# Optimization experiments

Measured on AMD Instinct MI355X. Metric: run time of the kernel, lower is better.

The kernel has to match this reference:

```python
import jax, jax.numpy as jnp
import numpy as np
import math

B, I, J = 4, 48, 384
D_TEXT, D_MEL, D_ATT = 512, 80, 128
NOISE_SCALE = 2.0
LOG_EPS = -1000.0


def setup_inputs() -> dict:
    key = jax.random.key(0)
    ks = jax.random.split(key, 8)
    return {
        "text_embeddings": jax.random.normal(ks[0], (B, I, D_TEXT), jnp.float32),
        "mel_embeddings": jax.random.normal(ks[1], (B, J, D_MEL), jnp.float32),
        "noise": jax.random.normal(ks[2], (B, I, J), jnp.float32),
        "W_text": jax.random.normal(ks[3], (D_TEXT, D_ATT), jnp.float32) * (1.0 / math.sqrt(D_TEXT)),
        "W_mel": jax.random.normal(ks[4], (D_MEL, D_ATT), jnp.float32) * (1.0 / math.sqrt(D_MEL)),
        "b_mel": jnp.zeros((D_ATT,), jnp.float32),
        "v_w": jax.random.normal(ks[5], (D_ATT,), jnp.float32) * math.sqrt(1.0 / D_ATT),
        "v_b": jnp.zeros((), jnp.float32),
        "text_mask": jnp.ones((B, I), bool),
        "mel_mask": jnp.ones((B, J), bool),
    }


def reference(text_embeddings, mel_embeddings, noise, W_text, W_mel, b_mel, v_w, v_b, text_mask, mel_mask):
    # ---- compute_energy: additive (Bahdanau) attention, v(tanh(Wt x_i + Wm m_j + b)) ----
    pt = text_embeddings @ W_text                    # (B,I,D_att), no bias
    pm = mel_embeddings @ W_mel + b_mel              # (B,J,D_att)
    energy = jnp.tanh(pt[:, :, None, :] + pm[:, None, :, :]) @ v_w + v_b   # (B,I,J)
    energy = energy + NOISE_SCALE * noise            # apply_noise

    tlen = text_mask.sum(1)                          # (B,)
    mlen = mel_mask.sum(1)                           # (B,)
    ii = jnp.arange(I)
    jj = jnp.arange(J)

    # ---- invalid mask for P(B_i = j | B_{i-1} = k): monotonic (j >= k), padding, force last ----
    inv = (jj[:, None] < jj[None, :])[None, None, :, :]                       # j < k invalid
    inv = inv | (~text_mask)[:, :, None, None]
    inv = inv | (~mel_mask)[:, None, :, None] | (~mel_mask)[:, None, None, :]
    last = (ii[None, :] == tlen[:, None] - 1)[:, :, None] & (jj[None, :] != mlen[:, None] - 1)[:, None, :]
    inv = inv | last[:, :, :, None]                                           # force_assign_last=True

    e4 = jnp.where(inv, LOG_EPS, energy[..., None])                           # (B,I,J,K)
    lcp = e4 - jax.nn.logsumexp(e4, axis=2, keepdims=True)                    # log P(j | i, k)
    geq = jax.lax.cumlogsumexp(lcp, axis=2, reverse=True)                     # log P(B_i >= j | k)
    geq = jnp.where(inv, LOG_EPS, geq)

    # ---- compute_forward_pass: banded DP over text positions (log domain) ----
    width = J - I + 2
    lcp_pad = jnp.concatenate([lcp, jnp.full((B, I, 1, J), LOG_EPS, lcp.dtype)], axis=2)  # (B,I,J+1,K)
    row0 = jnp.full((B, J + 1), -jnp.inf, lcp.dtype).at[:, 0].set(0.0)

    def step(prev, i):
        # B_ij[:, i, i : J-I+i+2] = LSE_k( B_ij[:, i-1, k] + lcp[:, i-1, i-1 : J-I+i+1, k] )
        blk = jax.lax.dynamic_slice(lcp_pad, (0, i - 1, i - 1, 0), (B, 1, width, J))[:, 0]  # (B,width,K)
        vals = jax.nn.logsumexp(prev[:, None, :-1] + blk, axis=2)                            # (B,width)
        row = jnp.full((B, J + 2), -jnp.inf, lcp.dtype)
        row = jax.lax.dynamic_update_slice(row, vals, (0, i))[:, :J + 1]
        return row, row

    _, rows = jax.lax.scan(step, row0, jnp.arange(1, I + 1))                  # (I,B,J+1)
    # Bij_forward = B_ij[:, :-1, :-1]
    Bij = jnp.concatenate([row0[:, None, :], jnp.moveaxis(rows, 0, 1)[:, :I - 1]], axis=1)[:, :, :-1]  # (B,I,J)

    # ---- compute_interval_probability: soft[b,i,j] = LSE_k( Bij[b,i,k] + geq[b,i,j,k] ) ----
    soft = jax.nn.logsumexp(Bij[:, :, None, :] + geq, axis=3)                 # (B,I,J)

    expanded = jnp.einsum('bij,bid->bjd', jnp.exp(soft), text_embeddings)     # (B,J,D_text)
    return soft, expanded
```

## Files before the change

### kernel.cpp

```cpp
#include <hip/hip_runtime.h>
#include <hip/hip_bf16.h>
#include <math.h>

#define B_ 4
#define I_ 48
#define J_ 384
#define DT_ 512
#define DM_ 80
#define DA_ 128
#define WIDTH_ 338
#define NEG (-1e30f)
#define LOG2E 1.4426950408889634f
#define LN2 0.6931471805599453f
#define LOGEPS2 (-1442.6950408889634f)
#define VPT 6

typedef float f32x4 __attribute__((ext_vector_type(4)));
typedef float f32x2 __attribute__((ext_vector_type(2)));

__device__ __forceinline__ float fexp2(float x) { return __builtin_amdgcn_exp2f(x); }
__device__ __forceinline__ float flog2(float x) { return __builtin_amdgcn_logf(x); }

template<int CTRL, int RMASK>
__device__ __forceinline__ float dppf(float x) {
    return __int_as_float(__builtin_amdgcn_update_dpp(
        __float_as_int(NEG), __float_as_int(x), CTRL, RMASK, 0xF, false));
}
__device__ __forceinline__ float rlane(float x, int l) {
    return __int_as_float(__builtin_amdgcn_readlane(__float_as_int(x), l));
}

__device__ __forceinline__ float lse2(float a, float b) {
    float m = fmaxf(a, b);
    float d = a - b;
    return m + flog2(1.0f + fexp2(-fabsf(d)));
}

__device__ __forceinline__ float wave_scan_fwd(float x) {
    x = lse2(x, dppf<0x111, 0xF>(x));
    x = lse2(x, dppf<0x112, 0xF>(x));
    x = lse2(x, dppf<0x114, 0xF>(x));
    x = lse2(x, dppf<0x118, 0xF>(x));
    x = lse2(x, dppf<0x142, 0xA>(x));
    x = lse2(x, dppf<0x143, 0xC>(x));
    return x;
}
__device__ __forceinline__ float wave_scan_rev(float x, int lane) {
    x = lse2(x, dppf<0x101, 0xF>(x));
    x = lse2(x, dppf<0x102, 0xF>(x));
    x = lse2(x, dppf<0x104, 0xF>(x));
    x = lse2(x, dppf<0x108, 0xF>(x));
    float s16 = rlane(x, 16), s32 = rlane(x, 32), s48 = rlane(x, 48);
    float a  = lse2(s32, s48);
    float b2 = lse2(s16, a);
    int row = lane >> 4;
    float pre = (row == 0) ? b2 : (row == 1) ? a : (row == 2) ? s48 : NEG;
    return lse2(x, pre);
}

__device__ __forceinline__ float tanh_fast(float x) {
    float t = fexp2(x * (2.0f * LOG2E));
    return fmaf(-2.0f, __builtin_amdgcn_rcpf(t + 1.0f), 1.0f);
}

__global__ __launch_bounds__(128) void proj_kernel(
        const float* __restrict__ text, const float* __restrict__ mel,
        const float* __restrict__ Wt, const float* __restrict__ Wm,
        const float* __restrict__ bm, float* __restrict__ pt, float* __restrict__ pm) {
    int blk = blockIdx.x;
    int d = threadIdx.x;
    __shared__ float sx[DT_];
    if (blk < B_ * I_) {
        const float* x = text + blk * DT_;
        for (int e = d; e < DT_; e += DA_) sx[e] = x[e];
        __syncthreads();
        float acc = 0.f;
        #pragma unroll 8
        for (int e = 0; e < DT_; ++e) acc += sx[e] * Wt[e * DA_ + d];
        pt[blk * DA_ + d] = acc;
    } else {
        int r = blk - B_ * I_;
        const float* x = mel + r * DM_;
        if (d < DM_) sx[d] = x[d];
        __syncthreads();
        float acc = bm[d];
        #pragma unroll 8
        for (int e = 0; e < DM_; ++e) acc += sx[e] * Wm[e * DA_ + d];
        pm[r * DA_ + d] = acc;
    }
}

__global__ __launch_bounds__(384) void energy_kernel(
        const float* __restrict__ pt, const float* __restrict__ pm,
        const float* __restrict__ vw, const float* __restrict__ vb,
        const float* __restrict__ noise, float* __restrict__ EZ) {
    int bi = blockIdx.x;
    int b = bi / I_, i = bi % I_;
    int t = threadIdx.x;
    int w = t >> 6, lane = t & 63;
    __shared__ float sPt[DA_];
    __shared__ float sPR[8];
    __shared__ float sLast;
    if (t < DA_) sPt[t] = pt[bi * DA_ + t];
    __syncthreads();
    const float4* pmr4 = (const float4*)(pm + (size_t)(b * J_ + t) * DA_);
    float acc = 0.f;
    #pragma unroll 8
    for (int q = 0; q < DA_ / 4; ++q) {
        float4 v = pmr4[q];
        acc += vw[4 * q + 0] * tanh_fast(sPt[4 * q + 0] + v.x);
        acc += vw[4 * q + 1] * tanh_fast(sPt[4 * q + 1] + v.y);
        acc += vw[4 * q + 2] * tanh_fast(sPt[4 * q + 2] + v.z);
        acc += vw[4 * q + 3] * tanh_fast(sPt[4 * q + 3] + v.w);
    }
    float e = (acc + vb[0] + 2.0f * noise[bi * J_ + t]) * LOG2E;

    float y = wave_scan_rev(e, lane);
    if (lane == 0) sPR[w] = y;
    if (t == J_ - 1) sLast = e;
    __syncthreads();
    float preR = NEG;
    #pragma unroll
    for (int ww = 1; ww < 6; ++ww) if (ww > w) preR = lse2(preR, sPR[ww]);
    float z = lse2(y, preR);
    if (i == I_ - 1) z = sLast;
    float2 o; o.x = e; o.y = z;
    ((float2*)(EZ + (size_t)bi * J_ * 2))[t] = o;
}

#define WAITV_(n) asm volatile("s_waitcnt vmcnt(" #n ")" ::: "memory")
#define WAITV(n) do { WAITV_(n); __builtin_amdgcn_sched_barrier(0); } while (0)

#define LOAD3(S, rowexpr) do { \
    const float* _a = EZb + (size_t)(rowexpr) * (2 * J_) + t * 12; \
    asm volatile("global_load_dwordx4 %0, %3, off\n\t" \
                 "global_load_dwordx4 %1, %3, off offset:16\n\t" \
                 "global_load_dwordx4 %2, %3, off offset:32" \
                 : "=&v"(S##0), "=&v"(S##1), "=&v"(S##2) \
                 : "v"(_a) : "memory"); } while (0)

#define STORE42(addr, q, dd) \
    asm volatile("global_store_dwordx4 %2, %0, off\n\t" \
                 "global_store_dwordx2 %2, %1, off offset:16" \
                 :: "v"(q), "v"(dd), "v"(addr) : "memory")

#define BODY(iexpr, NW, S, DOLOAD, lrow) do { \
    const int i_ = (iexpr); \
    WAITV(NW); \
    float e0 = S##0[0], z0 = S##0[1], e1 = S##0[2], z1 = S##0[3]; \
    float e2 = S##1[0], z2 = S##1[1], e3 = S##1[2], z3 = S##1[3]; \
    float e4 = S##2[0], z4 = S##2[1], e5 = S##2[2], z5 = S##2[3]; \
    if (DOLOAD) LOAD3(S, lrow); \
    float D0 = prev[0] - z0, D1 = prev[1] - z1, D2 = prev[2] - z2; \
    float D3 = prev[3] - z3, D4 = prev[4] - z4, D5 = prev[5] - z5; \
    float s01 = lse2(D0, D1), p23 = lse2(D2, D3), p45 = lse2(D4, D5); \
    float f2 = lse2(s01, D2), f3 = lse2(s01, p23); \
    float f4 = lse2(f3, D4),  f5 = lse2(f3, p45); \
    float Sf  = wave_scan_fwd(f5); \
    float exF = dppf<0x138, 0xF>(Sf);       \
    float flo = rlane(Sf, 63) + LOGEPS2;    \
    float eP  = dppf<0x138, 0xF>(e5);       \
    float v0 = lse2(eP + exF,         flo); \
    float v1 = lse2(e0 + lse2(D0,  exF), flo); \
    float v2 = lse2(e1 + lse2(s01, exF), flo); \
    float v3 = lse2(e2 + lse2(f2,  exF), flo); \
    float v4 = lse2(e3 + lse2(f3,  exF), flo); \
    float v5 = lse2(e4 + lse2(f4,  exF), flo); \
    int lo = i_, hi = i_ + WIDTH_; \
    prev[0] = (p0 + 0 >= lo && p0 + 0 < hi) ? v0 : NEG; \
    prev[1] = (p0 + 1 >= lo && p0 + 1 < hi) ? v1 : NEG; \
    prev[2] = (p0 + 2 >= lo && p0 + 2 < hi) ? v2 : NEG; \
    prev[3] = (p0 + 3 >= lo && p0 + 3 < hi) ? v3 : NEG; \
    prev[4] = (p0 + 4 >= lo && p0 + 4 < hi) ? v4 : NEG; \
    prev[5] = (p0 + 5 >= lo && p0 + 5 < hi) ? v5 : NEG; \
    { f32x4 q = {prev[0], prev[1], prev[2], prev[3]}; \
      f32x2 dd = {prev[4], prev[5]}; \
      float* _ba = Bb + i_ * J_ + p0; \
      STORE42(_ba, q, dd); } \
} while (0)

__global__ __launch_bounds__(64) void dp_kernel(
        const float* __restrict__ EZ, float* __restrict__ Bij) {
    int b = blockIdx.x;
    int t = threadIdx.x;
    int p0 = t * VPT;
    const float* EZb = EZ + (size_t)b * I_ * J_ * 2;
    float* Bb = Bij + b * I_ * J_;

    float prev[VPT];
    #pragma unroll
    for (int r = 0; r < VPT; ++r) prev[r] = (p0 + r == 0) ? 0.f : NEG;

    { f32x4 q = {prev[0], prev[1], prev[2], prev[3]};
      f32x2 dd = {prev[4], prev[5]};
      float* _ba = Bb + p0;
      STORE42(_ba, q, dd); }

    f32x4 A0, A1, A2, B0, B1, B2, C0, C1, C2;
    LOAD3(A, 0); LOAD3(B, 1); LOAD3(C, 2);

    BODY(1, 6,  A, 1, 3);
    BODY(2, 8,  B, 1, 4);
    BODY(3, 10, C, 1, 5);
    #pragma unroll 1
    for (int i = 4; i <= 43; i += 3) {
        BODY(i,     12, A, 1, i + 2);
        BODY(i + 1, 12, B, 1, i + 3);
        BODY(i + 2, 12, C, 1, i + 4);
    }
    BODY(46, 12, A, 0, 0);
    BODY(47, 9,  B, 0, 0);
}

__global__ __launch_bounds__(384) void soft_kernel(
        const float* __restrict__ Bij, const float* __restrict__ EZ,
        float* __restrict__ soft) {
    int bi = blockIdx.x;
    int i = bi % I_;
    int t = threadIdx.x;
    int w = t >> 6, lane = t & 63;
    __shared__ float sPF[8], sPR[8];
    float bv = Bij[bi * J_ + t];
    float2 ez = ((const float2*)(EZ + (size_t)bi * J_ * 2))[t];
    float zz = ez.y;

    float xf = wave_scan_fwd(bv - zz);
    float yr = wave_scan_rev(bv, lane);
    if (lane == 63) sPF[w] = xf;
    if (lane == 0)  sPR[w] = yr;
    __syncthreads();
    float preF = NEG, preR = NEG;
    #pragma unroll
    for (int ww = 0; ww < 5; ++ww) if (ww < w) preF = lse2(preF, sPF[ww]);
    #pragma unroll
    for (int ww = 1; ww < 6; ++ww) if (ww > w) preR = lse2(preR, sPR[ww]);

    float v;
    if (i < I_ - 1) {
        float cum   = lse2(xf, preF);
        float revp1 = lse2(dppf<0x130, 0xF>(yr), preR);
        v = lse2(zz + cum, revp1 + LOGEPS2);
    } else {
        float tot = lse2(lse2(lse2(sPR[0], sPR[1]), lse2(sPR[2], sPR[3])),
                         lse2(sPR[4], sPR[5]));
        v = (t == J_ - 1) ? tot : tot + LOGEPS2;
    }
    soft[bi * J_ + t] = v * LN2;
}

__global__ __launch_bounds__(512) void expand_kernel(
        const float* __restrict__ soft, const float* __restrict__ text,
        float* __restrict__ out) {
    int bj = blockIdx.x;
    int b = bj / J_, j = bj % J_;
    int d = threadIdx.x;
    __shared__ float p[I_];
    if (d < I_) p[d] = __expf(soft[(b * I_ + d) * J_ + j]);
    __syncthreads();
    float acc = 0.f;
    #pragma unroll
    for (int i = 0; i < I_; ++i) acc += p[i] * text[(b * I_ + i) * DT_ + d];
    out[bj * DT_ + d] = acc;
}

extern "C" void kernel_launch(void* const* d_in, const int* in_sizes, int n_in,
                              void* d_out, int out_size, void* d_ws, size_t ws_size,
                              hipStream_t stream) {
    const float* text  = (const float*)d_in[0];
    const float* mel   = (const float*)d_in[1];
    const float* noise = (const float*)d_in[2];
    const float* Wt    = (const float*)d_in[3];
    const float* Wm    = (const float*)d_in[4];
    const float* bm    = (const float*)d_in[5];
    const float* vw    = (const float*)d_in[6];
    const float* vb    = (const float*)d_in[7];

    float* ws  = (float*)d_ws;
    float* EZ  = ws;
    float* pt  = EZ + B_ * I_ * J_ * 2;
    float* pm  = pt + B_ * I_ * DA_;
    float* Bij = pm + B_ * J_ * DA_;

    float* soft     = (float*)d_out;
    float* expanded = soft + B_ * I_ * J_;

    proj_kernel<<<B_ * (I_ + J_), 128, 0, stream>>>(text, mel, Wt, Wm, bm, pt, pm);
    energy_kernel<<<B_ * I_, 384, 0, stream>>>(pt, pm, vw, vb, noise, EZ);
    dp_kernel<<<B_, 64, 0, stream>>>(EZ, Bij);
    soft_kernel<<<B_ * I_, 384, 0, stream>>>(Bij, EZ, soft);
    expand_kernel<<<B_ * J_, 512, 0, stream>>>(soft, text, expanded);
}
```

Baseline: 61.28 us.

## Fuse DP recursion and soft interval computation into one kernel via LDS ring

Merges the serial DP kernel and the soft-probability kernel into a single 384-thread block per batch. Wave 0 runs the DP recursion and writes each row of B and Z into a 4-deep shared-memory ring instead of global memory. Waves 1-5 compute the soft output of earlier rows concurrently, rotating rows among themselves. This removes one kernel launch and the global round-trip of Bij, but adds a __syncthreads on every DP step of the latency-critical serial chain and tightens the vmcnt waits.

```diff
diff --git a/kernel.cpp b/kernel.cpp
--- a/kernel.cpp
+++ b/kernel.cpp
@@ -16,7 +16,6 @@
 #define VPT 6
 
 typedef float f32x4 __attribute__((ext_vector_type(4)));
-typedef float f32x2 __attribute__((ext_vector_type(2)));
 
 __device__ __forceinline__ float fexp2(float x) { return __builtin_amdgcn_exp2f(x); }
 __device__ __forceinline__ float flog2(float x) { return __builtin_amdgcn_logf(x); }
@@ -128,6 +127,43 @@
     ((float2*)(EZ + (size_t)bi * J_ * 2))[t] = o;
 }
 
+__device__ __noinline__ void soft_row_fn(const float* rB, const float* rZ,
+                                         float* out, int lane, bool lastrow) {
+    int p0 = lane * VPT;
+    float Bv0 = rB[p0 + 0], Bv1 = rB[p0 + 1], Bv2 = rB[p0 + 2];
+    float Bv3 = rB[p0 + 3], Bv4 = rB[p0 + 4], Bv5 = rB[p0 + 5];
+    float q23 = lse2(Bv2, Bv3), q45 = lse2(Bv4, Bv5);
+    float g5 = Bv5, g4 = q45;
+    float g3 = lse2(Bv3, q45), g2 = lse2(q23, q45);
+    float g1 = lse2(Bv1, g2),  g0 = lse2(Bv0, g1);
+    float Sg = wave_scan_rev(g0, lane);
+    if (lastrow) {
+        float tot = rlane(Sg, 0);
+        #pragma unroll
+        for (int r = 0; r < VPT; ++r)
+            out[p0 + r] = ((p0 + r == J_ - 1) ? tot : tot + LOGEPS2) * LN2;
+        return;
+    }
+    float exG = dppf<0x130, 0xF>(Sg);
+    float Zv0 = rZ[p0 + 0], Zv1 = rZ[p0 + 1], Zv2 = rZ[p0 + 2];
+    float Zv3 = rZ[p0 + 3], Zv4 = rZ[p0 + 4], Zv5 = rZ[p0 + 5];
+    float C0 = Bv0 - Zv0, C1 = Bv1 - Zv1, C2 = Bv2 - Zv2;
+    float C3 = Bv3 - Zv3, C4 = Bv4 - Zv4, C5 = Bv5 - Zv5;
+    float s01 = lse2(C0, C1), p23 = lse2(C2, C3), p45 = lse2(C4, C5);
+    float f0 = C0, f1 = s01, f2 = lse2(s01, C2), f3 = lse2(s01, p23);
+    float f4 = lse2(f3, C4), f5 = lse2(f3, p45);
+    float Sf = wave_scan_fwd(f5);
+    float exF = dppf<0x138, 0xF>(Sf);
+    float o0 = lse2(Zv0 + lse2(f0, exF), lse2(g1, exG) + LOGEPS2);
+    float o1 = lse2(Zv1 + lse2(f1, exF), lse2(g2, exG) + LOGEPS2);
+    float o2 = lse2(Zv2 + lse2(f2, exF), lse2(g3, exG) + LOGEPS2);
+    float o3 = lse2(Zv3 + lse2(f3, exF), lse2(g4, exG) + LOGEPS2);
+    float o4 = lse2(Zv4 + lse2(f4, exF), lse2(g5, exG) + LOGEPS2);
+    float o5 = lse2(Zv5 + lse2(f5, exF), exG + LOGEPS2);
+    out[p0 + 0] = o0 * LN2; out[p0 + 1] = o1 * LN2; out[p0 + 2] = o2 * LN2;
+    out[p0 + 3] = o3 * LN2; out[p0 + 4] = o4 * LN2; out[p0 + 5] = o5 * LN2;
+}
+
 #define WAITV_(n) asm volatile("s_waitcnt vmcnt(" #n ")" ::: "memory")
 #define WAITV(n) do { WAITV_(n); __builtin_amdgcn_sched_barrier(0); } while (0)
 
@@ -139,11 +175,6 @@
                  : "=&v"(S##0), "=&v"(S##1), "=&v"(S##2) \
                  : "v"(_a) : "memory"); } while (0)
 
-#define STORE42(addr, q, dd) \
-    asm volatile("global_store_dwordx4 %2, %0, off\n\t" \
-                 "global_store_dwordx2 %2, %1, off offset:16" \
-                 :: "v"(q), "v"(dd), "v"(addr) : "memory")
-
 #define BODY(iexpr, NW, S, DOLOAD, lrow) do { \
     const int i_ = (iexpr); \
     WAITV(NW); \
@@ -151,6 +182,9 @@
     float e2 = S##1[0], z2 = S##1[1], e3 = S##1[2], z3 = S##1[3]; \
     float e4 = S##2[0], z4 = S##2[1], e5 = S##2[2], z5 = S##2[3]; \
     if (DOLOAD) LOAD3(S, lrow); \
+    ringZ[(i_ - 1) & 3][p0 + 0] = z0; ringZ[(i_ - 1) & 3][p0 + 1] = z1; \
+    ringZ[(i_ - 1) & 3][p0 + 2] = z2; ringZ[(i_ - 1) & 3][p0 + 3] = z3; \
+    ringZ[(i_ - 1) & 3][p0 + 4] = z4; ringZ[(i_ - 1) & 3][p0 + 5] = z5; \
     float D0 = prev[0] - z0, D1 = prev[1] - z1, D2 = prev[2] - z2; \
     float D3 = prev[3] - z3, D4 = prev[4] - z4, D5 = prev[5] - z5; \
     float s01 = lse2(D0, D1), p23 = lse2(D2, D3), p45 = lse2(D4, D5); \
@@ -160,7 +194,7 @@
     float exF = dppf<0x138, 0xF>(Sf);       \
     float flo = rlane(Sf, 63) + LOGEPS2;    \
     float eP  = dppf<0x138, 0xF>(e5);       \
-    float v0 = lse2(eP + exF,         flo); \
+    float v0 = lse2(eP + exF,            flo); \
     float v1 = lse2(e0 + lse2(D0,  exF), flo); \
     float v2 = lse2(e1 + lse2(s01, exF), flo); \
     float v3 = lse2(e2 + lse2(f2,  exF), flo); \
@@ -173,79 +207,68 @@
     prev[3] = (p0 + 3 >= lo && p0 + 3 < hi) ? v3 : NEG; \
     prev[4] = (p0 + 4 >= lo && p0 + 4 < hi) ? v4 : NEG; \
     prev[5] = (p0 + 5 >= lo && p0 + 5 < hi) ? v5 : NEG; \
-    { f32x4 q = {prev[0], prev[1], prev[2], prev[3]}; \
-      f32x2 dd = {prev[4], prev[5]}; \
-      float* _ba = Bb + i_ * J_ + p0; \
-      STORE42(_ba, q, dd); } \
+    ringB[i_ & 3][p0 + 0] = prev[0]; ringB[i_ & 3][p0 + 1] = prev[1]; \
+    ringB[i_ & 3][p0 + 2] = prev[2]; ringB[i_ & 3][p0 + 3] = prev[3]; \
+    ringB[i_ & 3][p0 + 4] = prev[4]; ringB[i_ & 3][p0 + 5] = prev[5]; \
 } while (0)
 
-__global__ __launch_bounds__(64) void dp_kernel(
-        const float* __restrict__ EZ, float* __restrict__ Bij) {
-    int b = blockIdx.x;
+#define ROUND(iexpr, NW, S, DOLOAD, lrow) do { \
+    if (t < 64) { BODY(iexpr, NW, S, DOLOAD, lrow); } \
+    else { \
+        int row_ = (iexpr) - 2; \
+        if (row_ >= 0 && w == 1 + (row_ % 5)) \
+            soft_row_fn(&ringB[row_ & 3][0], &ringZ[row_ & 3][0], \
+                        softB + (size_t)row_ * J_, lane, false); \
+    } \
+    __syncthreads(); \
+} while (0)
+
+__global__ __launch_bounds__(384) void dpsoft_kernel(
+        const float* __restrict__ EZ, float* __restrict__ soft) {
+    int blk = blockIdx.x;
     int t = threadIdx.x;
-    int p0 = t * VPT;
-    const float* EZb = EZ + (size_t)b * I_ * J_ * 2;
-    float* Bb = Bij + b * I_ * J_;
+    int w = t >> 6, lane = t & 63;
+    int p0 = lane * VPT;
+    const float* EZb = EZ + (size_t)blk * I_ * J_ * 2;
+    float* softB = soft + (size_t)blk * I_ * J_;
+
+    __shared__ float ringB[4][J_];
+    __shared__ float ringZ[4][J_];
 
     float prev[VPT];
-    #pragma unroll
-    for (int r = 0; r < VPT; ++r) prev[r] = (p0 + r == 0) ? 0.f : NEG;
-
-    { f32x4 q = {prev[0], prev[1], prev[2], prev[3]};
-      f32x2 dd = {prev[4], prev[5]};
-      float* _ba = Bb + p0;
-      STORE42(_ba, q, dd); }
-
     f32x4 A0, A1, A2, B0, B1, B2, C0, C1, C2;
-    LOAD3(A, 0); LOAD3(B, 1); LOAD3(C, 2);
-
-    BODY(1, 6,  A, 1, 3);
-    BODY(2, 8,  B, 1, 4);
-    BODY(3, 10, C, 1, 5);
+
+    if (t < 64) {
+        #pragma unroll
+        for (int r = 0; r < VPT; ++r) {
+            prev[r] = (p0 + r == 0) ? 0.f : NEG;
+            ringB[0][p0 + r] = prev[r];
+        }
+        LOAD3(A, 0); LOAD3(B, 1); LOAD3(C, 2);
+    }
+
+    ROUND(1, 6, A, 1, 3);
+    ROUND(2, 6, B, 1, 4);
+    ROUND(3, 6, C, 1, 5);
     #pragma unroll 1
     for (int i = 4; i <= 43; i += 3) {
-        BODY(i,     12, A, 1, i + 2);
-        BODY(i + 1, 12, B, 1, i + 3);
-        BODY(i + 2, 12, C, 1, i + 4);
-    }
-    BODY(46, 12, A, 0, 0);
-    BODY(47, 9,  B, 0, 0);
-}
-
-__global__ __launch_bounds__(384) void soft_kernel(
-        const float* __restrict__ Bij, const float* __restrict__ EZ,
-        float* __restrict__ soft) {
-    int bi = blockIdx.x;
-    int i = bi % I_;
-    int t = threadIdx.x;
-    int w = t >> 6, lane = t & 63;
-    __shared__ float sPF[8], sPR[8];
-    float bv = Bij[bi * J_ + t];
-    float2 ez = ((const float2*)(EZ + (size_t)bi * J_ * 2))[t];
-    float zz = ez.y;
-
-    float xf = wave_scan_fwd(bv - zz);
-    float yr = wave_scan_rev(bv, lane);
-    if (lane == 63) sPF[w] = xf;
-    if (lane == 0)  sPR[w] = yr;
-    __syncthreads();
-    float preF = NEG, preR = NEG;
-    #pragma unroll
-    for (int ww = 0; ww < 5; ++ww) if (ww < w) preF = lse2(preF, sPF[ww]);
-    #pragma unroll
-    for (int ww = 1; ww < 6; ++ww) if (ww > w) preR = lse2(preR, sPR[ww]);
-
-    float v;
-    if (i < I_ - 1) {
-        float cum   = lse2(xf, preF);
-        float revp1 = lse2(dppf<0x130, 0xF>(yr), preR);
-        v = lse2(zz + cum, revp1 + LOGEPS2);
-    } else {
-        float tot = lse2(lse2(lse2(sPR[0], sPR[1]), lse2(sPR[2], sPR[3])),
-                         lse2(sPR[4], sPR[5]));
-        v = (t == J_ - 1) ? tot : tot + LOGEPS2;
-    }
-    soft[bi * J_ + t] = v * LN2;
+        ROUND(i,     6, A, 1, i + 2);
+        ROUND(i + 1, 6, B, 1, i + 3);
+        ROUND(i + 2, 6, C, 1, i + 4);
+    }
+    ROUND(46, 6, A, 0, 0);
+    ROUND(47, 3, B, 0, 0);
+    {
+        int row_ = 46;
+        if (t >= 64 && w == 1 + (row_ % 5))
+            soft_row_fn(&ringB[row_ & 3][0], &ringZ[row_ & 3][0],
+                        softB + (size_t)row_ * J_, lane, false);
+        __syncthreads();
+        row_ = 47;
+        if (t >= 64 && w == 1 + (row_ % 5))
+            soft_row_fn(&ringB[row_ & 3][0], &ringB[row_ & 3][0],
+                        softB + (size_t)row_ * J_, lane, true);
+    }
 }
 
 __global__ __launch_bounds__(512) void expand_kernel(
@@ -279,14 +302,12 @@
     float* EZ  = ws;
     float* pt  = EZ + B_ * I_ * J_ * 2;
     float* pm  = pt + B_ * I_ * DA_;
-    float* Bij = pm + B_ * J_ * DA_;
 
     float* soft     = (float*)d_out;
     float* expanded = soft + B_ * I_ * J_;
 
     proj_kernel<<<B_ * (I_ + J_), 128, 0, stream>>>(text, mel, Wt, Wm, bm, pt, pm);
     energy_kernel<<<B_ * I_, 384, 0, stream>>>(pt, pm, vw, vb, noise, EZ);
-    dp_kernel<<<B_, 64, 0, stream>>>(EZ, Bij);
-    soft_kernel<<<B_ * I_, 384, 0, stream>>>(Bij, EZ, soft);
+    dpsoft_kernel<<<B_, 384, 0, stream>>>(EZ, soft);
     expand_kernel<<<B_ * J_, 512, 0, stream>>>(soft, text, expanded);
 }
```

Result: slower. 91.21 us (+48.8%).

## Fuse DP recursion and soft interval kernel into one per-batch block

Applied to the files above, without the earlier changes.

Merges the sequential DP kernel and the soft-probability kernel into a single 384-thread block per batch item. Wave 0 runs the recurrence, then after a barrier all six waves each handle eight rows of the soft computation, with six columns per lane. This removes one kernel launch and its inter-kernel gap. In exchange the soft stage runs on only four blocks instead of 192 and uses strided scalar loads.

```diff
diff --git a/kernel.cpp b/kernel.cpp
--- a/kernel.cpp
+++ b/kernel.cpp
@@ -160,7 +160,7 @@
     float exF = dppf<0x138, 0xF>(Sf);       \
     float flo = rlane(Sf, 63) + LOGEPS2;    \
     float eP  = dppf<0x138, 0xF>(e5);       \
-    float v0 = lse2(eP + exF,         flo); \
+    float v0 = lse2(eP + exF,            flo); \
     float v1 = lse2(e0 + lse2(D0,  exF), flo); \
     float v2 = lse2(e1 + lse2(s01, exF), flo); \
     float v3 = lse2(e2 + lse2(f2,  exF), flo); \
@@ -179,73 +179,85 @@
       STORE42(_ba, q, dd); } \
 } while (0)
 
-__global__ __launch_bounds__(64) void dp_kernel(
-        const float* __restrict__ EZ, float* __restrict__ Bij) {
-    int b = blockIdx.x;
-    int t = threadIdx.x;
-    int p0 = t * VPT;
-    const float* EZb = EZ + (size_t)b * I_ * J_ * 2;
-    float* Bb = Bij + b * I_ * J_;
-
-    float prev[VPT];
-    #pragma unroll
-    for (int r = 0; r < VPT; ++r) prev[r] = (p0 + r == 0) ? 0.f : NEG;
-
-    { f32x4 q = {prev[0], prev[1], prev[2], prev[3]};
-      f32x2 dd = {prev[4], prev[5]};
-      float* _ba = Bb + p0;
-      STORE42(_ba, q, dd); }
-
-    f32x4 A0, A1, A2, B0, B1, B2, C0, C1, C2;
-    LOAD3(A, 0); LOAD3(B, 1); LOAD3(C, 2);
-
-    BODY(1, 6,  A, 1, 3);
-    BODY(2, 8,  B, 1, 4);
-    BODY(3, 10, C, 1, 5);
-    #pragma unroll 1
-    for (int i = 4; i <= 43; i += 3) {
-        BODY(i,     12, A, 1, i + 2);
-        BODY(i + 1, 12, B, 1, i + 3);
-        BODY(i + 2, 12, C, 1, i + 4);
-    }
-    BODY(46, 12, A, 0, 0);
-    BODY(47, 9,  B, 0, 0);
-}
-
-__global__ __launch_bounds__(384) void soft_kernel(
-        const float* __restrict__ Bij, const float* __restrict__ EZ,
+__global__ __launch_bounds__(384) void dpsoft_kernel(
+        const float* __restrict__ EZ, float* __restrict__ Bij,
         float* __restrict__ soft) {
-    int bi = blockIdx.x;
-    int i = bi % I_;
+    int blk = blockIdx.x;
     int t = threadIdx.x;
     int w = t >> 6, lane = t & 63;
-    __shared__ float sPF[8], sPR[8];
-    float bv = Bij[bi * J_ + t];
-    float2 ez = ((const float2*)(EZ + (size_t)bi * J_ * 2))[t];
-    float zz = ez.y;
-
-    float xf = wave_scan_fwd(bv - zz);
-    float yr = wave_scan_rev(bv, lane);
-    if (lane == 63) sPF[w] = xf;
-    if (lane == 0)  sPR[w] = yr;
+    const float* EZb = EZ + (size_t)blk * I_ * J_ * 2;
+    float* Bb = Bij + (size_t)blk * I_ * J_;
+    float* softB = soft + (size_t)blk * I_ * J_;
+
+    if (t < 64) {
+        int p0 = t * VPT;
+        float prev[VPT];
+        #pragma unroll
+        for (int r = 0; r < VPT; ++r) prev[r] = (p0 + r == 0) ? 0.f : NEG;
+
+        { f32x4 q = {prev[0], prev[1], prev[2], prev[3]};
+          f32x2 dd = {prev[4], prev[5]};
+          float* _ba = Bb + p0;
+          STORE42(_ba, q, dd); }
+
+        f32x4 A0, A1, A2, B0, B1, B2, C0, C1, C2;
+        LOAD3(A, 0); LOAD3(B, 1); LOAD3(C, 2);
+
+        BODY(1, 6,  A, 1, 3);
+        BODY(2, 8,  B, 1, 4);
+        BODY(3, 10, C, 1, 5);
+        #pragma unroll 1
+        for (int i = 4; i <= 43; i += 3) {
+            BODY(i,     12, A, 1, i + 2);
+            BODY(i + 1, 12, B, 1, i + 3);
+            BODY(i + 2, 12, C, 1, i + 4);
+        }
+        BODY(46, 12, A, 0, 0);
+        BODY(47, 9,  B, 0, 0);
+    }
     __syncthreads();
-    float preF = NEG, preR = NEG;
-    #pragma unroll
-    for (int ww = 0; ww < 5; ++ww) if (ww < w) preF = lse2(preF, sPF[ww]);
-    #pragma unroll
-    for (int ww = 1; ww < 6; ++ww) if (ww > w) preR = lse2(preR, sPR[ww]);
-
-    float v;
-    if (i < I_ - 1) {
-        float cum   = lse2(xf, preF);
-        float revp1 = lse2(dppf<0x130, 0xF>(yr), preR);
-        v = lse2(zz + cum, revp1 + LOGEPS2);
-    } else {
-        float tot = lse2(lse2(lse2(sPR[0], sPR[1]), lse2(sPR[2], sPR[3])),
-                         lse2(sPR[4], sPR[5]));
-        v = (t == J_ - 1) ? tot : tot + LOGEPS2;
+
+    int p0 = lane * VPT;
+    #pragma unroll 1
+    for (int rr = 0; rr < 8; ++rr) {
+        int row = w * 8 + rr;
+        const float* Brow = Bb + (size_t)row * J_;
+        float Bv0 = Brow[p0 + 0], Bv1 = Brow[p0 + 1], Bv2 = Brow[p0 + 2];
+        float Bv3 = Brow[p0 + 3], Bv4 = Brow[p0 + 4], Bv5 = Brow[p0 + 5];
+        float q23 = lse2(Bv2, Bv3), q45 = lse2(Bv4, Bv5);
+        float g5 = Bv5, g4 = q45;
+        float g3 = lse2(Bv3, q45), g2 = lse2(q23, q45);
+        float g1 = lse2(Bv1, g2),  g0 = lse2(Bv0, g1);
+        float Sg = wave_scan_rev(g0, lane);
+        float* orow = softB + (size_t)row * J_ + p0;
+        if (row == I_ - 1) {
+            float tot = rlane(Sg, 0);
+            #pragma unroll
+            for (int r = 0; r < VPT; ++r)
+                orow[r] = ((p0 + r == J_ - 1) ? tot : tot + LOGEPS2) * LN2;
+        } else {
+            float exG = dppf<0x130, 0xF>(Sg);
+            const float* Erow = EZb + (size_t)row * 2 * J_;
+            float Zv0 = Erow[(p0 + 0) * 2 + 1], Zv1 = Erow[(p0 + 1) * 2 + 1];
+            float Zv2 = Erow[(p0 + 2) * 2 + 1], Zv3 = Erow[(p0 + 3) * 2 + 1];
+            float Zv4 = Erow[(p0 + 4) * 2 + 1], Zv5 = Erow[(p0 + 5) * 2 + 1];
+            float C0 = Bv0 - Zv0, C1 = Bv1 - Zv1, C2 = Bv2 - Zv2;
+            float C3 = Bv3 - Zv3, C4 = Bv4 - Zv4, C5 = Bv5 - Zv5;
+            float s01 = lse2(C0, C1), p23 = lse2(C2, C3), p45 = lse2(C4, C5);
+            float f0 = C0, f1 = s01, f2 = lse2(s01, C2), f3 = lse2(s01, p23);
+            float f4 = lse2(f3, C4), f5 = lse2(f3, p45);
+            float Sf = wave_scan_fwd(f5);
+            float exF = dppf<0x138, 0xF>(Sf);
+            float o0 = lse2(Zv0 + lse2(f0, exF), lse2(g1, exG) + LOGEPS2);
+            float o1 = lse2(Zv1 + lse2(f1, exF), lse2(g2, exG) + LOGEPS2);
+            float o2 = lse2(Zv2 + lse2(f2, exF), lse2(g3, exG) + LOGEPS2);
+            float o3 = lse2(Zv3 + lse2(f3, exF), lse2(g4, exG) + LOGEPS2);
+            float o4 = lse2(Zv4 + lse2(f4, exF), lse2(g5, exG) + LOGEPS2);
+            float o5 = lse2(Zv5 + lse2(f5, exF), exG + LOGEPS2);
+            orow[0] = o0 * LN2; orow[1] = o1 * LN2; orow[2] = o2 * LN2;
+            orow[3] = o3 * LN2; orow[4] = o4 * LN2; orow[5] = o5 * LN2;
+        }
     }
-    soft[bi * J_ + t] = v * LN2;
 }
 
 __global__ __launch_bounds__(512) void expand_kernel(
@@ -286,7 +298,6 @@
 
     proj_kernel<<<B_ * (I_ + J_), 128, 0, stream>>>(text, mel, Wt, Wm, bm, pt, pm);
     energy_kernel<<<B_ * I_, 384, 0, stream>>>(pt, pm, vw, vb, noise, EZ);
-    dp_kernel<<<B_, 64, 0, stream>>>(EZ, Bij);
-    soft_kernel<<<B_ * I_, 384, 0, stream>>>(Bij, EZ, soft);
+    dpsoft_kernel<<<B_, 384, 0, stream>>>(EZ, Bij, soft);
     expand_kernel<<<B_ * J_, 512, 0, stream>>>(soft, text, expanded);
 }
```

Measured after the change: 71.80 us. +17.2%, slower.
